# Optimization experiments

Hardware: AMD Instinct MI355X
Metric: run time of the kernel (lower is better)

The kernel has to match this reference:

```python
import jax, jax.numpy as jnp
import numpy as np

B, C, L = 4, 512, 4096
LN_EPS = 1e-5


def setup_inputs() -> dict:
    key = jax.random.key(0)
    ks = jax.random.split(key, 6)
    s = 1.0 / np.sqrt(C)
    return {
        "x": jax.random.normal(ks[0], (B, C, L), dtype=jnp.float32),
        "ln_w": jnp.ones((C,), dtype=jnp.float32),
        "ln_b": jnp.zeros((C,), dtype=jnp.float32),
        "wq": jax.random.normal(ks[1], (C, C), dtype=jnp.float32) * s,
        "bq": jnp.zeros((C,), dtype=jnp.float32),
        "wk": jax.random.normal(ks[2], (C, C), dtype=jnp.float32) * s,
        "bk": jnp.zeros((C,), dtype=jnp.float32),
        "wv": jax.random.normal(ks[3], (C, C), dtype=jnp.float32) * s,
        "bv": jnp.zeros((C,), dtype=jnp.float32),
        "wp": jax.random.normal(ks[4], (C, C), dtype=jnp.float32) * s,
        "bp": jnp.zeros((C,), dtype=jnp.float32),
    }


def reference(x, ln_w, ln_b, wq, bq, wk, bk, wv, bv, wp, bp):
    # x: [b, c, l]. LayerNorm over channels (permute -> LN -> permute back).
    xt = jnp.swapaxes(x, 1, 2)  # [b, l, c]
    mu = jnp.mean(xt, axis=-1, keepdims=True)
    var = jnp.var(xt, axis=-1, keepdims=True)
    h = (xt - mu) * jax.lax.rsqrt(var + LN_EPS) * ln_w + ln_b  # [b, l, c]

    # 1x1 convs == channel-mixing matmuls (weight [out, in])
    q = jnp.einsum('blc,oc->blo', h, wq) + bq  # [b, l, c]
    k = jnp.einsum('blc,oc->blo', h, wk) + bk
    v = jnp.einsum('blc,oc->blo', h, wv) + bv

    c = x.shape[1]
    scores = jnp.einsum('blc,bmc->blm', q, k) * (float(c) ** -0.5)  # [b, l_q, l_k]
    attn = jax.nn.softmax(scores, axis=-1)
    o = jnp.einsum('blm,bmc->blc', attn, v)  # [b, l, c]

    o = jnp.einsum('blc,oc->blo', o, wp) + bp
    o = jax.nn.selu(o)
    return x + jnp.swapaxes(o, 1, 2)  # [b, c, l]
```

## Files before the change

### kernel.cpp

```cpp
#include <hip/hip_runtime.h>


typedef __attribute__((ext_vector_type(8))) __bf16 bf16x8;
typedef __attribute__((ext_vector_type(4))) __bf16 bf16x4;
typedef __attribute__((ext_vector_type(4))) float  f32x4;

__device__ __forceinline__ f32x4 mfma16(bf16x8 a, bf16x8 b, f32x4 c) {
  return __builtin_amdgcn_mfma_f32_16x16x32_bf16(a, b, c, 0, 0, 0);
}

__device__ __forceinline__ void gll16(const void* g, void* l) {
  __builtin_amdgcn_global_load_lds(
      (const __attribute__((address_space(1))) unsigned int*)g,
      (__attribute__((address_space(3))) unsigned int*)l, 16, 0, 0);
}

__device__ __forceinline__ float selu_f(float v) {
  return 1.0507009873554805f * (v > 0.f ? v : 1.6732632423543772f * (__expf(v) - 1.f));
}

#define QSCALE ((float)(1.4426950408889634 / 22.627416997969522))

__global__ __launch_bounds__(256) void cvt_w(const float* __restrict__ w0,
                                             const float* __restrict__ w1,
                                             const float* __restrict__ w2,
                                             const float* __restrict__ w3,
                                             __bf16* __restrict__ dst) {
  int idx = blockIdx.x * 256 + threadIdx.x;
  int which = idx >> 16;
  const float* s = which == 0 ? w0 : which == 1 ? w1 : which == 2 ? w2 : w3;
  f32x4 v = *(const f32x4*)(s + (size_t)(idx & 65535) * 4);
  bf16x4 o = {(__bf16)v.x, (__bf16)v.y, (__bf16)v.z, (__bf16)v.w};
  *(bf16x4*)(dst + (size_t)idx * 4) = o;
}

__global__ __launch_bounds__(256) void ln_fused(const float* __restrict__ x,
                                                const float* __restrict__ lw,
                                                const float* __restrict__ lb,
                                                __bf16* __restrict__ h) {
  __shared__ float red[16][16][4][2];
  __shared__ float smu[64], srs[64];
  __shared__ float t2[64][65];
  const int b = blockIdx.y, l0 = blockIdx.x * 64;
  const int tid = threadIdx.x;
  const int hi = tid >> 4, lq = tid & 15;

  {
    const float* xp = x + (size_t)b * 2097152 + l0 + lq * 4;
    float s[4] = {0.f, 0.f, 0.f, 0.f}, qq[4] = {0.f, 0.f, 0.f, 0.f};
    for (int it = 0; it < 32; ++it) {
      int c = it * 16 + hi;
      f32x4 v = *(const f32x4*)(xp + (size_t)c * 4096);
#pragma unroll
      for (int k = 0; k < 4; ++k) { s[k] += v[k]; qq[k] += v[k] * v[k]; }
    }
#pragma unroll
    for (int k = 0; k < 4; ++k) {
      red[hi][lq][k][0] = s[k];
      red[hi][lq][k][1] = qq[k];
    }
  }
  __syncthreads();
  if (tid < 64) {
    int lqq = tid >> 2, k = tid & 3;
    float S = 0.f, Q = 0.f;
    for (int hh = 0; hh < 16; ++hh) {
      S += red[hh][lqq][k][0];
      Q += red[hh][lqq][k][1];
    }
    float m = S * (1.f / 512.f);
    float var = Q * (1.f / 512.f) - m * m;
    smu[lqq * 4 + k] = m;
    srs[lqq * 4 + k] = rsqrtf(var + 1e-5f);
  }
  __syncthreads();

  const int li = tid & 63, r4 = tid >> 6;
  for (int cb = 0; cb < 8; ++cb) {
    int c0 = cb * 64;
    const float* xq = x + (size_t)(b * 512 + c0) * 4096 + l0;
#pragma unroll
    for (int rr = 0; rr < 16; ++rr) {
      int cl = rr * 4 + r4;
      t2[cl][li] = xq[(size_t)cl * 4096 + li];
    }
    __syncthreads();
    float gw = lw[c0 + li], gb = lb[c0 + li];
#pragma unroll
    for (int rr = 0; rr < 16; ++rr) {
      int lr = rr * 4 + r4;
      float v = (t2[li][lr] - smu[lr]) * srs[lr] * gw + gb;
      h[((size_t)b * 4096 + l0 + lr) * 512 + c0 + li] = (__bf16)v;
    }
    __syncthreads();
  }
}

__global__ __launch_bounds__(256, 2) void gemm_qkv(
    const __bf16* __restrict__ A, const __bf16* __restrict__ W,
    const float* __restrict__ b0, const float* __restrict__ b1,
    const float* __restrict__ b2, __bf16* __restrict__ out,
    __bf16* __restrict__ vt) {
  __shared__ __align__(16) __bf16 smem[2 * 128 * 128];
  __bf16* As = smem;
  __bf16* Bs = smem + 16384;
  const int tid = threadIdx.x;
  const int w = tid >> 6, lane = tid & 63, g = lane >> 4, li = lane & 15;
  const int id = blockIdx.x;
  const int jj = id >> 3;
  const int m0 = (16 * (id & 7) + jj / 12) * 128;
  const int n0 = (jj % 12) * 128;
  const int wm = w >> 1, wn = w & 1;
  const int srow = lane >> 4;
  f32x4 acc[4][4] = {};
  for (int kt = 0; kt < 4; ++kt) {
    __syncthreads();
#pragma unroll
    for (int qq = 0; qq < 8; ++qq) {
      int r = w * 32 + qq * 4;
      int gr = (lane & 15) ^ (4 * (qq & 1) + srow);
      gll16(A + (size_t)(m0 + r + srow) * 512 + kt * 128 + gr * 8, &As[r * 128]);
      gll16(W + (size_t)(n0 + r + srow) * 512 + kt * 128 + gr * 8, &Bs[r * 128]);
    }
    __syncthreads();
#pragma unroll
    for (int kk = 0; kk < 4; ++kk) {
      bf16x8 af[4], bf[4];
#pragma unroll
      for (int t = 0; t < 4; ++t) {
        int ra = wm * 64 + t * 16 + li;
        af[t] = *(const bf16x8*)&As[ra * 128 + ((kk * 32 + 8 * g) ^ ((ra & 7) * 8))];
        int rb = wn * 64 + t * 16 + li;
        bf[t] = *(const bf16x8*)&Bs[rb * 128 + ((kk * 32 + 8 * g) ^ ((rb & 7) * 8))];
      }
#pragma unroll
      for (int i = 0; i < 4; ++i)
#pragma unroll
        for (int j = 0; j < 4; ++j) acc[i][j] = mfma16(af[i], bf[j], acc[i][j]);
    }
  }
  const int which = n0 >> 9;
  __syncthreads();
  if (which < 2) {
    const float* bb = which == 0 ? b0 : b1;
    const float sc = which == 0 ? QSCALE : 1.0f;
#pragma unroll
    for (int i = 0; i < 4; ++i) {
#pragma unroll
      for (int j = 0; j < 4; ++j) {
        int rl = wm * 64 + i * 16 + 4 * g;
        int cl = wn * 64 + j * 16 + li;
        float bv = bb[(n0 & 511) + cl];
#pragma unroll
        for (int e = 0; e < 4; ++e)
          smem[(rl + e) * 128 + cl] = (__bf16)((acc[i][j][e] + bv) * sc);
      }
    }
    __syncthreads();
    __bf16* o = out + (size_t)which * 8388608;
#pragma unroll
    for (int rep = 0; rep < 8; ++rep) {
      int ii = rep * 256 + tid;
      int row = ii >> 4, col8 = (ii & 15) * 8;
      *(bf16x8*)&o[(size_t)(m0 + row) * 512 + (n0 & 511) + col8] =
          *(const bf16x8*)&smem[row * 128 + col8];
    }
  } else {
#pragma unroll
    for (int i = 0; i < 4; ++i) {
#pragma unroll
      for (int j = 0; j < 4; ++j) {
        int rl = wm * 64 + i * 16 + 4 * g;
        int cl = wn * 64 + j * 16 + li;
        float bv = b2[(n0 & 511) + cl];
        bf16x4 pk = {(__bf16)(acc[i][j][0] + bv), (__bf16)(acc[i][j][1] + bv),
                     (__bf16)(acc[i][j][2] + bv), (__bf16)(acc[i][j][3] + bv)};
        *(bf16x4*)&smem[cl * 136 + rl] = pk;
      }
    }
    __syncthreads();
    const int bb_ = m0 >> 12, l0_ = m0 & 4095;
#pragma unroll
    for (int rep = 0; rep < 8; ++rep) {
      int chan = rep * 16 + (tid >> 4);
      int l8 = (tid & 15) * 8;
      *(bf16x8*)&vt[((size_t)(bb_ * 512) + (n0 & 511) + chan) * 4096 + l0_ + l8] =
          *(const bf16x8*)&smem[chan * 136 + l8];
    }
  }
}

__global__ __launch_bounds__(256, 2) void gemm_pp(
    const __bf16* __restrict__ A, const __bf16* __restrict__ Bm,
    const float* __restrict__ bias, const float* __restrict__ xres,
    float* __restrict__ out) {
  __shared__ __align__(16) __bf16 As[128 * 128];
  __shared__ __align__(16) __bf16 Bs[128 * 128];
  const int tid = threadIdx.x;
  const int w = tid >> 6, lane = tid & 63, g = lane >> 4, li = lane & 15;
  const int id = blockIdx.x;
  const int jj = id >> 3;
  const int n0 = (16 * (id & 7) + (jj & 15)) * 128;
  const int m0 = (jj >> 4) * 128;
  const int wm = w >> 1, wn = w & 1;
  const int srow = lane >> 4;
  f32x4 acc[4][4] = {};
  for (int kt = 0; kt < 4; ++kt) {
    __syncthreads();
#pragma unroll
    for (int qq = 0; qq < 8; ++qq) {
      int r = w * 32 + qq * 4;
      int gr = (lane & 15) ^ (4 * (qq & 1) + srow);
      gll16(A + (size_t)(m0 + r + srow) * 512 + kt * 128 + gr * 8, &As[r * 128]);
      gll16(Bm + (size_t)(n0 + r + srow) * 512 + kt * 128 + gr * 8, &Bs[r * 128]);
    }
    __syncthreads();
#pragma unroll
    for (int kk = 0; kk < 4; ++kk) {
      bf16x8 af[4], bf[4];
#pragma unroll
      for (int t = 0; t < 4; ++t) {
        int ra = wm * 64 + t * 16 + li;
        af[t] = *(const bf16x8*)&As[ra * 128 + ((kk * 32 + 8 * g) ^ ((ra & 7) * 8))];
        int rb = wn * 64 + t * 16 + li;
        bf[t] = *(const bf16x8*)&Bs[rb * 128 + ((kk * 32 + 8 * g) ^ ((rb & 7) * 8))];
      }
#pragma unroll
      for (int i = 0; i < 4; ++i)
#pragma unroll
        for (int j = 0; j < 4; ++j) acc[i][j] = mfma16(af[i], bf[j], acc[i][j]);
    }
  }
#pragma unroll
  for (int i = 0; i < 4; ++i) {
#pragma unroll
    for (int j = 0; j < 4; ++j) {
      int r = m0 + wm * 64 + i * 16 + 4 * g;
      int c = n0 + wn * 64 + j * 16 + li;
      int bb = c >> 12, l = c & 4095;
#pragma unroll
      for (int e = 0; e < 4; ++e) {
        float v = acc[i][j][e] + bias[r + e];
        size_t oi = ((size_t)bb * 512 + (r + e)) * 4096 + l;
        out[oi] = xres[oi] + selu_f(v);
      }
    }
  }
}

__global__ __launch_bounds__(512, 2) void flash_half(
    const __bf16* __restrict__ Q, const __bf16* __restrict__ K,
    const __bf16* __restrict__ VT, __bf16* __restrict__ Op,
    float* __restrict__ stats) {
  __shared__ __align__(16) __bf16 Ks[64][512];
  __shared__ __align__(16) __bf16 VTs[512][64];
  __shared__ __align__(16) __bf16 Ps[128][64];

  const int tid = threadIdx.x;
  const int w = tid >> 6, lane = tid & 63, g = lane >> 4, li = lane & 15;
  const int id = blockIdx.x;
  const int grp = id & 7;
  const int b = grp >> 1, half = grp & 1;
  const int q0 = (id >> 3) * 128;
  const size_t base = (size_t)b * (4096 * 512);
  const int kvbase = half * 2048;

  bf16x8 qf[16];
  {
    const __bf16* qp = Q + base + (size_t)(q0 + 16 * w + li) * 512 + 8 * g;
#pragma unroll
    for (int ks = 0; ks < 16; ++ks) qf[ks] = *(const bf16x8*)(qp + ks * 32);
  }

  f32x4 acc[8][4] = {};
  f32x4 lacc = {};
  bf16x8 ones;
#pragma unroll
  for (int j = 0; j < 8; ++j) ones[j] = (__bf16)1.0f;

  auto stageK = [&](int kt) {
#pragma unroll
    for (int i = 0; i < 8; ++i) {
      int r = w * 8 + i;
      int y = (lane * 16) ^ ((r & 7) << 4);
      gll16(K + base + (size_t)(kvbase + kt * 64 + r) * 512 + (y >> 1),
            &Ks[r][0]);
    }
  };
  auto stageVT = [&](int kt) {
    const int drow = lane >> 3;
    const int gr = (lane & 7) ^ drow;
#pragma unroll
    for (int i = 0; i < 8; ++i) {
      int d0 = w * 64 + i * 8;
      gll16(VT + (size_t)b * 2097152 + (size_t)(d0 + drow) * 4096 +
                kvbase + kt * 64 + gr * 8,
            &VTs[d0][0]);
    }
  };

  stageK(0);
  stageVT(0);
  __syncthreads();

  for (int kt = 0; kt < 32; ++kt) {
    __builtin_amdgcn_s_setprio(1);
    f32x4 s[4] = {};
#pragma unroll
    for (int ks = 0; ks < 16; ++ks) {
      int e = (ks * 32 + 8 * g) ^ ((li & 7) * 8);
#pragma unroll
      for (int kvt = 0; kvt < 4; ++kvt) {
        bf16x8 kf = *(const bf16x8*)&Ks[kvt * 16 + li][e];
        s[kvt] = mfma16(qf[ks], kf, s[kvt]);
      }
    }
    __builtin_amdgcn_s_setprio(0);

#pragma unroll
    for (int kvt = 0; kvt < 4; ++kvt) {
#pragma unroll
      for (int e = 0; e < 4; ++e) {
        float p = exp2f(s[kvt][e]);
        int row = 16 * w + 4 * g + e;
        int slot = (2 * kvt + (li >> 3)) ^ (row & 7);
        Ps[row][slot * 8 + (li & 7)] = (__bf16)p;
      }
    }
    __syncthreads();

    if (kt + 1 < 32) stageK(kt + 1);

#pragma unroll
    for (int ks = 0; ks < 2; ++ks) {
      bf16x8 bfr[4];
#pragma unroll
      for (int ct = 0; ct < 4; ++ct) {
        int dcol = 64 * w + 16 * ct + li;
        int slot = (4 * ks + g) ^ (li & 7);
        bfr[ct] = *(const bf16x8*)&VTs[dcol][slot * 8];
      }
      __builtin_amdgcn_s_setprio(1);
#pragma unroll
      for (int rt = 0; rt < 8; ++rt) {
        int prow = rt * 16 + li;
        int slot = (4 * ks + g) ^ (li & 7);
        bf16x8 af = *(const bf16x8*)&Ps[prow][slot * 8];
        if (rt == w) lacc = mfma16(af, ones, lacc);
#pragma unroll
        for (int ct = 0; ct < 4; ++ct)
          acc[rt][ct] = mfma16(af, bfr[ct], acc[rt][ct]);
      }
      __builtin_amdgcn_s_setprio(0);
    }
    __syncthreads();

    if (kt + 1 < 32) stageVT(kt + 1);
  }

  if (li == 0)
    *(f32x4*)(stats + half * 16384 + b * 4096 + q0 + 16 * w + 4 * g) = lacc;

  __bf16* C = &Ps[0][0];
  for (int rt = 0; rt < 8; ++rt) {
    __syncthreads();
#pragma unroll
    for (int ct = 0; ct < 4; ++ct)
#pragma unroll
      for (int e = 0; e < 4; ++e)
        C[(4 * g + e) * 512 + 64 * w + 16 * ct + li] = (__bf16)acc[rt][ct][e];
    __syncthreads();
#pragma unroll
    for (int rep = 0; rep < 2; ++rep) {
      int ii = rep * 512 + tid;
      int row16 = ii >> 6, col8 = (ii & 63) * 8;
      *(bf16x8*)&Op[(size_t)half * 8388608 + base +
                    (size_t)(q0 + rt * 16 + row16) * 512 + col8] =
          *(const bf16x8*)&C[row16 * 512 + col8];
    }
  }
}

__global__ __launch_bounds__(256) void combine2(const __bf16* __restrict__ Op,
                                                const float* __restrict__ stats,
                                                __bf16* __restrict__ ao) {
  int gid = blockIdx.x * 256 + threadIdx.x;
  int row = gid >> 6;
  int c = (gid & 63) * 8;
  float l0 = stats[row], l1 = stats[16384 + row];
  float inv = 1.f / (l0 + l1);
  bf16x8 v0 = *(const bf16x8*)(Op + (size_t)row * 512 + c);
  bf16x8 v1 = *(const bf16x8*)(Op + 8388608 + (size_t)row * 512 + c);
  bf16x8 o;
#pragma unroll
  for (int j = 0; j < 8; ++j)
    o[j] = (__bf16)(((float)v0[j] + (float)v1[j]) * inv);
  *(bf16x8*)(ao + (size_t)row * 512 + c) = o;
}

extern "C" void kernel_launch(void* const* d_in, const int* in_sizes, int n_in,
                              void* d_out, int out_size, void* d_ws, size_t ws_size,
                              hipStream_t stream) {
  const float* x   = (const float*)d_in[0];
  const float* lnw = (const float*)d_in[1];
  const float* lnb = (const float*)d_in[2];
  const float* wq  = (const float*)d_in[3];
  const float* bq  = (const float*)d_in[4];
  const float* wk  = (const float*)d_in[5];
  const float* bk  = (const float*)d_in[6];
  const float* wv  = (const float*)d_in[7];
  const float* bv  = (const float*)d_in[8];
  const float* wp  = (const float*)d_in[9];
  const float* bp  = (const float*)d_in[10];

  char* ws = (char*)d_ws;
  const size_t MB = 1024 * 1024;
  __bf16* h    = (__bf16*)(ws);
  __bf16* q    = (__bf16*)(ws + 16 * MB);
  __bf16* vt   = (__bf16*)(ws + 48 * MB);
  __bf16* wbf  = (__bf16*)(ws + 64 * MB);
  __bf16* op   = (__bf16*)(ws + 67 * MB);
  float*  stats= (float*)(ws + 99 * MB);
  __bf16* ao   = h;

  cvt_w<<<1024, 256, 0, stream>>>(wq, wk, wv, wp, wbf);
  ln_fused<<<dim3(64, 4), 256, 0, stream>>>(x, lnw, lnb, h);
  gemm_qkv<<<1536, 256, 0, stream>>>(h, wbf, bq, bk, bv, q, vt);
  flash_half<<<256, 512, 0, stream>>>(q, q + 8388608, vt, op, stats);
  combine2<<<4096, 256, 0, stream>>>(op, stats, ao);
  gemm_pp<<<512, 256, 0, stream>>>(wbf + 3 * 262144, ao, bp, x,
                                   (float*)d_out);
}
```

Baseline: 288.8 us.

## Fuse weight conversion into LayerNorm kernel and cache x tile in LDS

Merges the weight-to-bf16 conversion and the LayerNorm kernels into one launch, with extra blocks doing the weight conversion. The LayerNorm part now handles 32 positions per block and keeps the whole 512x32 x tile in shared memory after the statistics pass, so x is read from global memory once instead of twice. This removes one kernel launch and half of the x traffic, at the cost of a large shared-memory footprint (about 66 KB) that limits blocks per CU, plus strided LDS reads in the normalize loop.

```diff
diff --git a/kernel.cpp b/kernel.cpp
--- a/kernel.cpp
+++ b/kernel.cpp
@@ -21,38 +21,43 @@
 
 #define QSCALE ((float)(1.4426950408889634 / 22.627416997969522))
 
-__global__ __launch_bounds__(256) void cvt_w(const float* __restrict__ w0,
-                                             const float* __restrict__ w1,
-                                             const float* __restrict__ w2,
-                                             const float* __restrict__ w3,
-                                             __bf16* __restrict__ dst) {
-  int idx = blockIdx.x * 256 + threadIdx.x;
-  int which = idx >> 16;
-  const float* s = which == 0 ? w0 : which == 1 ? w1 : which == 2 ? w2 : w3;
-  f32x4 v = *(const f32x4*)(s + (size_t)(idx & 65535) * 4);
-  bf16x4 o = {(__bf16)v.x, (__bf16)v.y, (__bf16)v.z, (__bf16)v.w};
-  *(bf16x4*)(dst + (size_t)idx * 4) = o;
-}
-
-__global__ __launch_bounds__(256) void ln_fused(const float* __restrict__ x,
-                                                const float* __restrict__ lw,
-                                                const float* __restrict__ lb,
-                                                __bf16* __restrict__ h) {
-  __shared__ float red[16][16][4][2];
-  __shared__ float smu[64], srs[64];
-  __shared__ float t2[64][65];
-  const int b = blockIdx.y, l0 = blockIdx.x * 64;
-  const int tid = threadIdx.x;
-  const int hi = tid >> 4, lq = tid & 15;
+__global__ __launch_bounds__(256) void ln_cvt(
+    const float* __restrict__ x, const float* __restrict__ lw,
+    const float* __restrict__ lb, __bf16* __restrict__ h,
+    const float* __restrict__ w0, const float* __restrict__ w1,
+    const float* __restrict__ w2, const float* __restrict__ w3,
+    __bf16* __restrict__ wdst) {
+  __shared__ float xf[512][33];
+  __shared__ float red[32][8][4][2];
+  __shared__ float smu[32], srs[32];
+  const int id = blockIdx.x, tid = threadIdx.x;
+
+  if (id >= 512) {
+    int idx = (id - 512) * 256 + tid;
+    int which = idx >> 16;
+    const float* s = which == 0 ? w0 : which == 1 ? w1 : which == 2 ? w2 : w3;
+    f32x4 v = *(const f32x4*)(s + (size_t)(idx & 65535) * 4);
+    bf16x4 o = {(__bf16)v.x, (__bf16)v.y, (__bf16)v.z, (__bf16)v.w};
+    *(bf16x4*)(wdst + (size_t)idx * 4) = o;
+    return;
+  }
+
+  const int b = id >> 7, l0 = (id & 127) * 32;
+  const int hi = tid >> 3, lq = tid & 7;
 
   {
     const float* xp = x + (size_t)b * 2097152 + l0 + lq * 4;
     float s[4] = {0.f, 0.f, 0.f, 0.f}, qq[4] = {0.f, 0.f, 0.f, 0.f};
-    for (int it = 0; it < 32; ++it) {
-      int c = it * 16 + hi;
+#pragma unroll
+    for (int it = 0; it < 16; ++it) {
+      int c = it * 32 + hi;
       f32x4 v = *(const f32x4*)(xp + (size_t)c * 4096);
 #pragma unroll
-      for (int k = 0; k < 4; ++k) { s[k] += v[k]; qq[k] += v[k] * v[k]; }
+      for (int k = 0; k < 4; ++k) {
+        s[k] += v[k];
+        qq[k] += v[k] * v[k];
+        xf[c][lq * 4 + k] = v[k];
+      }
     }
 #pragma unroll
     for (int k = 0; k < 4; ++k) {
@@ -61,38 +66,30 @@
     }
   }
   __syncthreads();
-  if (tid < 64) {
-    int lqq = tid >> 2, k = tid & 3;
+  if (tid < 32) {
+    int l4 = tid >> 2, k = tid & 3;
     float S = 0.f, Q = 0.f;
-    for (int hh = 0; hh < 16; ++hh) {
-      S += red[hh][lqq][k][0];
-      Q += red[hh][lqq][k][1];
+#pragma unroll
+    for (int hh = 0; hh < 32; ++hh) {
+      S += red[hh][l4][k][0];
+      Q += red[hh][l4][k][1];
     }
     float m = S * (1.f / 512.f);
     float var = Q * (1.f / 512.f) - m * m;
-    smu[lqq * 4 + k] = m;
-    srs[lqq * 4 + k] = rsqrtf(var + 1e-5f);
+    smu[tid] = m;
+    srs[tid] = rsqrtf(var + 1e-5f);
   }
   __syncthreads();
 
-  const int li = tid & 63, r4 = tid >> 6;
-  for (int cb = 0; cb < 8; ++cb) {
-    int c0 = cb * 64;
-    const float* xq = x + (size_t)(b * 512 + c0) * 4096 + l0;
-#pragma unroll
-    for (int rr = 0; rr < 16; ++rr) {
-      int cl = rr * 4 + r4;
-      t2[cl][li] = xq[(size_t)cl * 4096 + li];
-    }
-    __syncthreads();
-    float gw = lw[c0 + li], gb = lb[c0 + li];
-#pragma unroll
-    for (int rr = 0; rr < 16; ++rr) {
-      int lr = rr * 4 + r4;
-      float v = (t2[li][lr] - smu[lr]) * srs[lr] * gw + gb;
-      h[((size_t)b * 4096 + l0 + lr) * 512 + c0 + li] = (__bf16)v;
-    }
-    __syncthreads();
+#pragma unroll
+  for (int l = 0; l < 32; ++l) {
+    float m = smu[l], r = srs[l];
+#pragma unroll
+    for (int st = 0; st < 2; ++st) {
+      int c = st * 256 + tid;
+      float v = (xf[c][l] - m) * r * lw[c] + lb[c];
+      h[((size_t)b * 4096 + l0 + l) * 512 + c] = (__bf16)v;
+    }
   }
 }
 
@@ -423,8 +420,7 @@
   float*  stats= (float*)(ws + 99 * MB);
   __bf16* ao   = h;
 
-  cvt_w<<<1024, 256, 0, stream>>>(wq, wk, wv, wp, wbf);
-  ln_fused<<<dim3(64, 4), 256, 0, stream>>>(x, lnw, lnb, h);
+  ln_cvt<<<1536, 256, 0, stream>>>(x, lnw, lnb, h, wq, wk, wv, wp, wbf);
   gemm_qkv<<<1536, 256, 0, stream>>>(h, wbf, bq, bk, bv, q, vt);
   flash_half<<<256, 512, 0, stream>>>(q, q + 8388608, vt, op, stats);
   combine2<<<4096, 256, 0, stream>>>(op, stats, ao);
```

Result: faster. 280.8 us (-2.8%).
